# Kernel optimization log

Measured on AMD Instinct MI355X. Metric: run time of the kernel, lower is better.

## Reference

```python
import jax, jax.numpy as jnp
import numpy as np

N = 50000
E = 800000
IN, HID, OUT = 256, 128, 64
NEG_SLOPE = 0.2


def _gat(x, src, dst, W, a_src, a_dst, b, heads, dim, concat):
    # PyG GATConv (eval mode, self-loops already appended to src/dst)
    xh = (x @ W).reshape(N, heads, dim)              # [N,H,D]
    s_src = jnp.einsum('nhd,hd->nh', xh, a_src)       # [N,H]
    s_dst = jnp.einsum('nhd,hd->nh', xh, a_dst)
    e = jax.nn.leaky_relu(s_src[src] + s_dst[dst], NEG_SLOPE)  # [Etot,H]
    m = jax.ops.segment_max(e, dst, num_segments=N)
    e = jnp.exp(e - m[dst])
    z = jax.ops.segment_sum(e, dst, num_segments=N)
    alpha = e / z[dst]                                # segment softmax over incoming edges
    msg = xh[src] * alpha[:, :, None]                 # [Etot,H,D] gather + weight
    out = jax.ops.segment_sum(msg, dst, num_segments=N)  # scatter-add aggregate
    out = out.reshape(N, heads * dim) if concat else out.mean(axis=1)
    return out + b


def setup_inputs():
    key = jax.random.key(0)
    ks = jax.random.split(key, 20)
    sc = 0.05
    inp = {
        'x': jax.random.normal(ks[0], (N, IN), jnp.float32),
        'edge_index': jax.random.randint(ks[1], (2, E), 0, N, jnp.int64) if jax.config.read('jax_enable_x64') else jax.random.randint(ks[1], (2, E), 0, N, jnp.int32),
        # semantic MLP
        'w1': jax.random.normal(ks[2], (IN, HID), jnp.float32) * sc,
        'b1': jnp.zeros((HID,), jnp.float32),
        'w2': jax.random.normal(ks[3], (HID, HID), jnp.float32) * sc,
        'b2': jnp.zeros((HID,), jnp.float32),
        # gat1: HID -> HID//2, heads=4, concat -> 2*HID
        'g1_w': jax.random.normal(ks[4], (HID, 4 * (HID // 2)), jnp.float32) * sc,
        'g1_asrc': jax.random.normal(ks[5], (4, HID // 2), jnp.float32) * sc,
        'g1_adst': jax.random.normal(ks[6], (4, HID // 2), jnp.float32) * sc,
        'g1_b': jnp.zeros((2 * HID,), jnp.float32),
        # gat2: 2*HID -> OUT, heads=2, mean
        'g2_w': jax.random.normal(ks[7], (2 * HID, 2 * OUT), jnp.float32) * sc,
        'g2_asrc': jax.random.normal(ks[8], (2, OUT), jnp.float32) * sc,
        'g2_adst': jax.random.normal(ks[9], (2, OUT), jnp.float32) * sc,
        'g2_b': jnp.zeros((OUT,), jnp.float32),
        # gat3: OUT -> OUT, heads=1, mean
        'g3_w': jax.random.normal(ks[10], (OUT, OUT), jnp.float32) * sc,
        'g3_asrc': jax.random.normal(ks[11], (1, OUT), jnp.float32) * sc,
        'g3_adst': jax.random.normal(ks[12], (1, OUT), jnp.float32) * sc,
        'g3_b': jnp.zeros((OUT,), jnp.float32),
    }
    return inp


def reference(x, edge_index, w1, b1, w2, b2,
              g1_w, g1_asrc, g1_adst, g1_b,
              g2_w, g2_asrc, g2_adst, g2_b,
              g3_w, g3_asrc, g3_adst, g3_b):
    # add self loops once (PyG GATConv default add_self_loops=True)
    loop = jnp.arange(N, dtype=edge_index.dtype)
    src = jnp.concatenate([edge_index[0], loop])
    dst = jnp.concatenate([edge_index[1], loop])
    # semantic MLP (eval: dropout is identity)
    h = jax.nn.relu(x @ w1 + b1)
    h = jax.nn.relu(h @ w2 + b2)
    h = jax.nn.elu(_gat(h, src, dst, g1_w, g1_asrc, g1_adst, g1_b, 4, HID // 2, True))
    h = jax.nn.elu(_gat(h, src, dst, g2_w, g2_asrc, g2_adst, g2_b, 2, OUT, False))
    h = _gat(h, src, dst, g3_w, g3_asrc, g3_adst, g3_b, 1, OUT, False)
    return h
```

## Files before the change

kernel.cpp:

```cpp
#include <hip/hip_runtime.h>
#include <hip/hip_fp16.h>
#include <math.h>

#define NN 50000
#define NE 800000

static inline int ceil_div_h(int a, int b) { return (a + b - 1) / b; }

typedef _Float16 half8 __attribute__((ext_vector_type(8)));
typedef float f32x4 __attribute__((ext_vector_type(4)));

__global__ __launch_bounds__(256)
void convert_all_kernel(const float* __restrict__ w1, const float* __restrict__ w2,
                        const float* __restrict__ g1w, const float* __restrict__ g2w,
                        const float* __restrict__ g3w, __half* __restrict__ wt) {
  int idx = blockIdx.x * 256 + threadIdx.x;
  const float* W; int K, N, li;
  if (idx < 32768)        { W = w1;  K = 256; N = 128; li = idx; }
  else if (idx < 49152)   { W = w2;  K = 128; N = 128; li = idx - 32768; }
  else if (idx < 81920)   { W = g1w; K = 128; N = 256; li = idx - 49152; }
  else if (idx < 114688)  { W = g2w; K = 256; N = 128; li = idx - 81920; }
  else if (idx < 118784)  { W = g3w; K = 64;  N = 64;  li = idx - 114688; }
  else return;
  int n = li / K, k = li - n * K;
  wt[idx] = __float2half_rn(W[(size_t)k * N + n]);
}

template<int TN, int ACT, int OUTH, int AF32, int HS>
__global__ __launch_bounds__(256)
void mfma_gemm(const void* __restrict__ Av, const __half* __restrict__ Bt,
               const float* __restrict__ bias, void* __restrict__ Cv,
               const float* __restrict__ a_src, const float* __restrict__ a_dst,
               float* __restrict__ s_src, float* __restrict__ s_dst,
               int M, int N, int K) {
  constexpr int FM = 4;
  constexpr int FN = TN / 32;
  constexpr int SA = 40;
  __shared__ __align__(16) _Float16 As[128 * SA];
  __shared__ __align__(16) _Float16 Bs[TN * SA];
  const int tid = threadIdx.x;
  const int bm = blockIdx.y * 128, bn = blockIdx.x * TN;
  const int wave = tid >> 6, lane = tid & 63;
  const int wm = (wave & 1) * 64;
  const int wn = (wave >> 1) * (TN / 2);
  const int l16 = lane & 15, quad = lane >> 4;

  f32x4 acc[FM][FN] = {};

  for (int k0 = 0; k0 < K; k0 += 32) {
    if (AF32) {
      const float* A = (const float*)Av;
      #pragma unroll
      for (int i = 0; i < 4; ++i) {
        int idx = tid + i * 256;
        int m = idx >> 3, q = idx & 7;
        int gm = bm + m;
        float4 v = make_float4(0.f, 0.f, 0.f, 0.f);
        if (gm < M) v = *(const float4*)&A[(size_t)gm * K + k0 + q * 4];
        union { __half2 h2[2]; float2 f2; } u;
        u.h2[0] = __floats2half2_rn(v.x, v.y);
        u.h2[1] = __floats2half2_rn(v.z, v.w);
        *(float2*)&As[m * SA + q * 4] = u.f2;
      }
    } else {
      const __half* A = (const __half*)Av;
      #pragma unroll
      for (int i = 0; i < 2; ++i) {
        int idx = tid + i * 256;
        int m = idx >> 2, q = (idx & 3) * 8;
        int gm = bm + m;
        float4 raw = make_float4(0.f, 0.f, 0.f, 0.f);
        if (gm < M) raw = *(const float4*)&A[(size_t)gm * K + k0 + q];
        *(float4*)&As[m * SA + q] = raw;
      }
    }
    #pragma unroll
    for (int i = 0; i < (TN * 32) / (256 * 8); ++i) {
      int idx = tid + i * 256;
      int n = idx >> 2, kq = (idx & 3) * 8;
      float4 raw = *(const float4*)&Bt[(size_t)(bn + n) * K + k0 + kq];
      *(float4*)&Bs[n * SA + kq] = raw;
    }
    __syncthreads();
    half8 af[FM], bf[FN];
    #pragma unroll
    for (int mi = 0; mi < FM; ++mi)
      af[mi] = *(const half8*)&As[(wm + mi * 16 + l16) * SA + quad * 8];
    #pragma unroll
    for (int ni = 0; ni < FN; ++ni)
      bf[ni] = *(const half8*)&Bs[(wn + ni * 16 + l16) * SA + quad * 8];
    #pragma unroll
    for (int mi = 0; mi < FM; ++mi)
      #pragma unroll
      for (int ni = 0; ni < FN; ++ni)
        acc[mi][ni] = __builtin_amdgcn_mfma_f32_16x16x32_f16(af[mi], bf[ni], acc[mi][ni], 0, 0, 0);
    __syncthreads();
  }

  #pragma unroll
  for (int mi = 0; mi < FM; ++mi) {
    #pragma unroll
    for (int r = 0; r < 4; ++r) {
      int gm = bm + wm + mi * 16 + quad * 4 + r;
      if (gm >= M) continue;
      #pragma unroll
      for (int ni = 0; ni < FN; ++ni) {
        int gn = bn + wn + ni * 16 + l16;
        float v = acc[mi][ni][r];
        if (bias) v += bias[gn];
        if (ACT == 1) v = fmaxf(v, 0.f);
        if (OUTH) ((__half*)Cv)[(size_t)gm * N + gn] = __float2half_rn(v);
        else      ((float*)Cv)[(size_t)gm * N + gn] = v;
      }
    }
  }

  if (HS > 0) {
    const int h = (bn + wn) >> 6;
    float asv[FN], adv[FN];
    #pragma unroll
    for (int ni = 0; ni < FN; ++ni) {
      int d = ni * 16 + l16;
      asv[ni] = a_src[h * 64 + d];
      adv[ni] = a_dst[h * 64 + d];
    }
    #pragma unroll
    for (int mi = 0; mi < FM; ++mi) {
      #pragma unroll
      for (int r = 0; r < 4; ++r) {
        float ss = 0.f, sd = 0.f;
        #pragma unroll
        for (int ni = 0; ni < FN; ++ni) {
          float v = acc[mi][ni][r];
          ss = fmaf(v, asv[ni], ss);
          sd = fmaf(v, adv[ni], sd);
        }
        #pragma unroll
        for (int off = 1; off < 16; off <<= 1) {
          ss += __shfl_xor(ss, off, 64);
          sd += __shfl_xor(sd, off, 64);
        }
        int gm = bm + wm + mi * 16 + quad * 4 + r;
        if (l16 == 0 && gm < M) {
          s_src[gm * HS + h] = ss;
          s_dst[gm * HS + h] = sd;
        }
      }
    }
  }
}

template<int H>
__global__ __launch_bounds__(256)
void scores_kernel(const __half* __restrict__ xh,
                   const float* __restrict__ a_src, const float* __restrict__ a_dst,
                   float* __restrict__ s_src, float* __restrict__ s_dst) {
  const int n = (blockIdx.x * blockDim.x + threadIdx.x) >> 6;
  const int lane = threadIdx.x & 63;
  if (n >= NN) return;
  float ps[H], pd[H];
  #pragma unroll
  for (int h = 0; h < H; ++h) {
    float v = __half2float(xh[(size_t)n * (H * 64) + h * 64 + lane]);
    ps[h] = v * a_src[h * 64 + lane];
    pd[h] = v * a_dst[h * 64 + lane];
  }
  #pragma unroll
  for (int h = 0; h < H; ++h) {
    #pragma unroll
    for (int off = 32; off > 0; off >>= 1) {
      ps[h] += __shfl_xor(ps[h], off, 64);
      pd[h] += __shfl_xor(pd[h], off, 64);
    }
  }
  if (lane == 0) {
    #pragma unroll
    for (int h = 0; h < H; ++h) {
      s_src[n * H + h] = ps[h];
      s_dst[n * H + h] = pd[h];
    }
  }
}


__global__ __launch_bounds__(256)
void hist_kernel(const int* __restrict__ ei, int* __restrict__ cnt) {
  int e = blockIdx.x * blockDim.x + threadIdx.x;
  if (e >= NE) return;
  atomicAdd(&cnt[ei[NE + e]], 1);
}

__global__ __launch_bounds__(256)
void scan1_kernel(const int* __restrict__ in, int* __restrict__ out,
                  int* __restrict__ bsum, int n) {
  __shared__ int tmp[256];
  int t = threadIdx.x;
  int i = blockIdx.x * 256 + t;
  int v = (i < n) ? in[i] : 0;
  tmp[t] = v;
  __syncthreads();
  for (int off = 1; off < 256; off <<= 1) {
    int u = (t >= off) ? tmp[t - off] : 0;
    __syncthreads();
    tmp[t] += u;
    __syncthreads();
  }
  if (i <= n) out[i] = tmp[t] - v;
  if (t == 255) bsum[blockIdx.x] = tmp[255];
}

__global__ __launch_bounds__(256)
void scan2_kernel(int* __restrict__ data, int n) {
  __shared__ int tmp[256];
  int t = threadIdx.x;
  int v = (t < n) ? data[t] : 0;
  tmp[t] = v;
  __syncthreads();
  for (int off = 1; off < 256; off <<= 1) {
    int u = (t >= off) ? tmp[t - off] : 0;
    __syncthreads();
    tmp[t] += u;
    __syncthreads();
  }
  if (t < n) data[t] = tmp[t] - v;
}

__global__ __launch_bounds__(256)
void scan3_kernel(int* __restrict__ out, const int* __restrict__ bsum, int n) {
  int i = blockIdx.x * 256 + threadIdx.x;
  if (i <= n) out[i] += bsum[blockIdx.x];
}

__global__ __launch_bounds__(256)
void copy_cursor_kernel(const int* __restrict__ rowptr, int* __restrict__ cursor) {
  int i = blockIdx.x * blockDim.x + threadIdx.x;
  if (i < NN) cursor[i] = rowptr[i];
}

__global__ __launch_bounds__(256)
void scatter_kernel(const int* __restrict__ ei, int* __restrict__ cursor,
                    int* __restrict__ srcs) {
  int e = blockIdx.x * blockDim.x + threadIdx.x;
  if (e >= NE) return;
  int s = ei[e], d = ei[NE + e];
  int pos = atomicAdd(&cursor[d], 1);
  srcs[pos] = s;
}

template<int H, int MODE>
__global__ __launch_bounds__(256)
void gat_aggregate(const int* __restrict__ rowptr, const int* __restrict__ srcs,
                   const float* __restrict__ ssrc, const float* __restrict__ sdst,
                   const __half* __restrict__ xh, const float* __restrict__ bias,
                   void* __restrict__ outv) {
  constexpr int HD = H * 64;
  __shared__ float wbuf[4][64 * H];
  __shared__ int sbuf[4][64];
  const int wslot = threadIdx.x >> 6;
  const int wid = (blockIdx.x * blockDim.x + threadIdx.x) >> 6;
  const int lane = threadIdx.x & 63;
  if (wid >= NN) return;
  const int n = wid;
  const int start = rowptr[n];
  const int end = rowptr[n + 1];
  const int h = (lane * H) >> 6;

  float sdv[H];
  #pragma unroll
  for (int hh = 0; hh < H; ++hh) sdv[hh] = sdst[n * H + hh];

  float z;
  float acc[H];
  {
    float wself[H];
    #pragma unroll
    for (int hh = 0; hh < H; ++hh) {
      float e = ssrc[n * H + hh] + sdv[hh];
      e = e >= 0.f ? e : 0.2f * e;
      wself[hh] = __expf(e);
    }
    float ws = wself[h];
    z = ws;
    const __half* xr = xh + (size_t)n * HD + lane * H;
    if (H == 4) {
      float2 raw = *(const float2*)xr;
      __half2 p0 = *(__half2*)&raw.x;
      __half2 p1 = *(__half2*)&raw.y;
      float2 f0 = __half22float2(p0), f1 = __half22float2(p1);
      acc[0] = ws * f0.x; acc[1] = ws * f0.y; acc[2] = ws * f1.x; acc[3] = ws * f1.y;
    } else if (H == 2) {
      float2 f0 = __half22float2(*(const __half2*)xr);
      acc[0] = ws * f0.x; acc[1] = ws * f0.y;
    } else {
      acc[0] = ws * __half2float(xr[0]);
    }
  }

  for (int base = start; base < end; base += 64) {
    int cnt = end - base;
    if (cnt > 64) cnt = 64;
    if (lane < cnt) {
      int s = srcs[base + lane];
      sbuf[wslot][lane] = s;
      float ev[H];
      if (H == 4) {
        float4 t = *(const float4*)&ssrc[s * 4];
        ev[0] = t.x; ev[1] = t.y; ev[2] = t.z; ev[3] = t.w;
      } else if (H == 2) {
        float2 t = *(const float2*)&ssrc[s * 2];
        ev[0] = t.x; ev[1] = t.y;
      } else {
        ev[0] = ssrc[s];
      }
      #pragma unroll
      for (int hh = 0; hh < H; ++hh) {
        float e = ev[hh] + sdv[hh];
        e = e >= 0.f ? e : 0.2f * e;
        wbuf[wslot][lane * H + hh] = __expf(e);
      }
    }
    #pragma unroll 4
    for (int j = 0; j < cnt; ++j) {
      int s = sbuf[wslot][j];
      float w = wbuf[wslot][j * H + h];
      z += w;
      const __half* xr = xh + (size_t)s * HD + lane * H;
      if (H == 4) {
        float2 raw = *(const float2*)xr;
        __half2 p0 = *(__half2*)&raw.x;
        __half2 p1 = *(__half2*)&raw.y;
        float2 f0 = __half22float2(p0), f1 = __half22float2(p1);
        acc[0] = fmaf(w, f0.x, acc[0]); acc[1] = fmaf(w, f0.y, acc[1]);
        acc[2] = fmaf(w, f1.x, acc[2]); acc[3] = fmaf(w, f1.y, acc[3]);
      } else if (H == 2) {
        float2 f0 = __half22float2(*(const __half2*)xr);
        acc[0] = fmaf(w, f0.x, acc[0]); acc[1] = fmaf(w, f0.y, acc[1]);
      } else {
        acc[0] = fmaf(w, __half2float(xr[0]), acc[0]);
      }
    }
  }
  const float inv = 1.f / z;

  if (MODE == 0) {
    __half* out = (__half*)outv;
    float v[4];
    #pragma unroll
    for (int i = 0; i < 4; ++i) {
      v[i] = acc[i] * inv + bias[lane * 4 + i];
      v[i] = v[i] > 0.f ? v[i] : expm1f(v[i]);
    }
    union { __half2 h2[2]; float2 f2; } u;
    u.h2[0] = __floats2half2_rn(v[0], v[1]);
    u.h2[1] = __floats2half2_rn(v[2], v[3]);
    *(float2*)&out[(size_t)n * 256 + lane * 4] = u.f2;
  } else if (MODE == 1) {
    __half* out = (__half*)outv;
    float sv[2];
    #pragma unroll
    for (int i = 0; i < 2; ++i) {
      float mine = acc[i] * inv;
      float other = __shfl_xor(mine, 32, 64);
      sv[i] = (mine + other) * 0.5f;
    }
    if (lane < 32) {
      float v0 = sv[0] + bias[lane * 2 + 0];
      float v1 = sv[1] + bias[lane * 2 + 1];
      v0 = v0 > 0.f ? v0 : expm1f(v0);
      v1 = v1 > 0.f ? v1 : expm1f(v1);
      *(__half2*)&out[(size_t)n * 64 + lane * 2] = __floats2half2_rn(v0, v1);
    }
  } else {
    float* out = (float*)outv;
    out[(size_t)n * 64 + lane] = acc[0] * inv + bias[lane];
  }
}


extern "C" void kernel_launch(void* const* d_in, const int* in_sizes, int n_in,
                              void* d_out, int out_size, void* d_ws, size_t ws_size,
                              hipStream_t stream) {
  const float* x    = (const float*)d_in[0];
  const int*   ei   = (const int*)d_in[1];
  const float* w1   = (const float*)d_in[2];
  const float* b1   = (const float*)d_in[3];
  const float* w2   = (const float*)d_in[4];
  const float* b2   = (const float*)d_in[5];
  const float* g1w  = (const float*)d_in[6];
  const float* g1as = (const float*)d_in[7];
  const float* g1ad = (const float*)d_in[8];
  const float* g1b  = (const float*)d_in[9];
  const float* g2w  = (const float*)d_in[10];
  const float* g2as = (const float*)d_in[11];
  const float* g2ad = (const float*)d_in[12];
  const float* g2b  = (const float*)d_in[13];
  const float* g3w  = (const float*)d_in[14];
  const float* g3as = (const float*)d_in[15];
  const float* g3ad = (const float*)d_in[16];
  const float* g3b  = (const float*)d_in[17];
  float* out = (float*)d_out;

  float* ws   = (float*)d_ws;
  float* bufA = ws;
  float* bufB = bufA + (size_t)NN * 256;
  float* bufC = bufB + (size_t)NN * 256;
  float* ssrc = bufC + (size_t)NN * 256;
  float* sdst = ssrc + (size_t)NN * 4;
  int* rowptr = (int*)(sdst + (size_t)NN * 4);
  int* cursor = rowptr + (NN + 1);
  int* bsum   = cursor + NN;
  int* srcs   = bsum + 256;
  __half* wt   = (__half*)(srcs + NE);
  __half* wt1  = wt;
  __half* wt2  = wt + 32768;
  __half* wtg1 = wt + 49152;
  __half* wtg2 = wt + 81920;
  __half* wtg3 = wt + 114688;

  __half* h1  = (__half*)bufA;
  __half* h2  = (__half*)bufB;
  __half* xh1 = (__half*)bufC;
  __half* a1  = (__half*)bufA;
  __half* xh2 = (__half*)bufB;
  __half* a2  = (__half*)bufC;
  __half* xh3 = (__half*)bufB;

  const int TB = 256;
  const int grid_m = ceil_div_h(NN, 128);
  const int egrid = ceil_div_h(NE, TB);
  const int sgrid = ceil_div_h(NN + 1, TB);
  const int wgrid = ceil_div_h(NN, 4);

  convert_all_kernel<<<ceil_div_h(118784, TB), TB, 0, stream>>>(w1, w2, g1w, g2w, g3w, wt);

  hipMemsetAsync(cursor, 0, (size_t)NN * sizeof(int), stream);
  hist_kernel<<<egrid, TB, 0, stream>>>(ei, cursor);
  scan1_kernel<<<sgrid, TB, 0, stream>>>(cursor, rowptr, bsum, NN);
  scan2_kernel<<<1, TB, 0, stream>>>(bsum, sgrid);
  scan3_kernel<<<sgrid, TB, 0, stream>>>(rowptr, bsum, NN);
  copy_cursor_kernel<<<ceil_div_h(NN, TB), TB, 0, stream>>>(rowptr, cursor);
  scatter_kernel<<<egrid, TB, 0, stream>>>(ei, cursor, srcs);

  mfma_gemm<128, 1, 1, 1, 0><<<dim3(1, grid_m), TB, 0, stream>>>(
      x, wt1, b1, h1, nullptr, nullptr, nullptr, nullptr, NN, 128, 256);
  mfma_gemm<128, 1, 1, 0, 0><<<dim3(1, grid_m), TB, 0, stream>>>(
      h1, wt2, b2, h2, nullptr, nullptr, nullptr, nullptr, NN, 128, 128);

  mfma_gemm<128, 0, 1, 0, 4><<<dim3(2, grid_m), TB, 0, stream>>>(
      h2, wtg1, nullptr, xh1, g1as, g1ad, ssrc, sdst, NN, 256, 128);
  gat_aggregate<4, 0><<<wgrid, TB, 0, stream>>>(rowptr, srcs, ssrc, sdst, xh1, g1b, a1);

  mfma_gemm<128, 0, 1, 0, 2><<<dim3(1, grid_m), TB, 0, stream>>>(
      a1, wtg2, nullptr, xh2, g2as, g2ad, ssrc, sdst, NN, 128, 256);
  gat_aggregate<2, 1><<<wgrid, TB, 0, stream>>>(rowptr, srcs, ssrc, sdst, xh2, g2b, a2);

  mfma_gemm<64, 0, 1, 0, 0><<<dim3(1, grid_m), TB, 0, stream>>>(
      a2, wtg3, nullptr, xh3, nullptr, nullptr, nullptr, nullptr, NN, 64, 64);
  scores_kernel<1><<<wgrid, TB, 0, stream>>>(xh3, g3as, g3ad, ssrc, sdst);
  gat_aggregate<1, 2><<<wgrid, TB, 0, stream>>>(rowptr, srcs, ssrc, sdst, xh3, g3b, out);
}
```

Baseline: 457.8 us.

## Shrink GEMM row tiles, fuse layer-3 scores into GEMM, merge prep kernels

Makes the MFMA GEMM template take its block-M and wave layout as parameters and switches every GEMM to 64-row tiles, doubling the grid for better CU occupancy. The third-layer score computation moves into the GEMM epilogue (HS=1), which removes the separate scores kernel. The cursor memset is folded into the weight conversion kernel, and the cursor copy is folded into scan3, cutting launch count. Smaller tiles re-read the B operand more often per output row.

```diff
diff --git a/kernel.cpp b/kernel.cpp
--- a/kernel.cpp
+++ b/kernel.cpp
@@ -11,10 +11,12 @@
 typedef float f32x4 __attribute__((ext_vector_type(4)));
 
 __global__ __launch_bounds__(256)
-void convert_all_kernel(const float* __restrict__ w1, const float* __restrict__ w2,
-                        const float* __restrict__ g1w, const float* __restrict__ g2w,
-                        const float* __restrict__ g3w, __half* __restrict__ wt) {
+void prep_kernel(const float* __restrict__ w1, const float* __restrict__ w2,
+                 const float* __restrict__ g1w, const float* __restrict__ g2w,
+                 const float* __restrict__ g3w, __half* __restrict__ wt,
+                 int* __restrict__ cursor) {
   int idx = blockIdx.x * 256 + threadIdx.x;
+  if (idx < NN) cursor[idx] = 0;
   const float* W; int K, N, li;
   if (idx < 32768)        { W = w1;  K = 256; N = 128; li = idx; }
   else if (idx < 49152)   { W = w2;  K = 128; N = 128; li = idx - 32768; }
@@ -26,23 +28,23 @@
   wt[idx] = __float2half_rn(W[(size_t)k * N + n]);
 }
 
-template<int TN, int ACT, int OUTH, int AF32, int HS>
+template<int BM, int TN, int WR, int WC, int ACT, int OUTH, int AF32, int HS>
 __global__ __launch_bounds__(256)
 void mfma_gemm(const void* __restrict__ Av, const __half* __restrict__ Bt,
                const float* __restrict__ bias, void* __restrict__ Cv,
                const float* __restrict__ a_src, const float* __restrict__ a_dst,
                float* __restrict__ s_src, float* __restrict__ s_dst,
                int M, int N, int K) {
-  constexpr int FM = 4;
-  constexpr int FN = TN / 32;
+  constexpr int FM = BM / WR / 16;
+  constexpr int FN = TN / WC / 16;
   constexpr int SA = 40;
-  __shared__ __align__(16) _Float16 As[128 * SA];
+  __shared__ __align__(16) _Float16 As[BM * SA];
   __shared__ __align__(16) _Float16 Bs[TN * SA];
   const int tid = threadIdx.x;
-  const int bm = blockIdx.y * 128, bn = blockIdx.x * TN;
+  const int bm = blockIdx.y * BM, bn = blockIdx.x * TN;
   const int wave = tid >> 6, lane = tid & 63;
-  const int wm = (wave & 1) * 64;
-  const int wn = (wave >> 1) * (TN / 2);
+  const int wm = (wave % WR) * (BM / WR);
+  const int wn = (wave / WR) * (TN / WC);
   const int l16 = lane & 15, quad = lane >> 4;
 
   f32x4 acc[FM][FN] = {};
@@ -51,7 +53,7 @@
     if (AF32) {
       const float* A = (const float*)Av;
       #pragma unroll
-      for (int i = 0; i < 4; ++i) {
+      for (int i = 0; i < (BM * 8) / 256; ++i) {
         int idx = tid + i * 256;
         int m = idx >> 3, q = idx & 7;
         int gm = bm + m;
@@ -65,7 +67,7 @@
     } else {
       const __half* A = (const __half*)Av;
       #pragma unroll
-      for (int i = 0; i < 2; ++i) {
+      for (int i = 0; i < (BM * 4) / 256; ++i) {
         int idx = tid + i * 256;
         int m = idx >> 2, q = (idx & 3) * 8;
         int gm = bm + m;
@@ -75,7 +77,7 @@
       }
     }
     #pragma unroll
-    for (int i = 0; i < (TN * 32) / (256 * 8); ++i) {
+    for (int i = 0; i < (TN * 4) / 256; ++i) {
       int idx = tid + i * 256;
       int n = idx >> 2, kq = (idx & 3) * 8;
       float4 raw = *(const float4*)&Bt[(size_t)(bn + n) * K + k0 + kq];
@@ -150,38 +152,6 @@
   }
 }
 
-template<int H>
-__global__ __launch_bounds__(256)
-void scores_kernel(const __half* __restrict__ xh,
-                   const float* __restrict__ a_src, const float* __restrict__ a_dst,
-                   float* __restrict__ s_src, float* __restrict__ s_dst) {
-  const int n = (blockIdx.x * blockDim.x + threadIdx.x) >> 6;
-  const int lane = threadIdx.x & 63;
-  if (n >= NN) return;
-  float ps[H], pd[H];
-  #pragma unroll
-  for (int h = 0; h < H; ++h) {
-    float v = __half2float(xh[(size_t)n * (H * 64) + h * 64 + lane]);
-    ps[h] = v * a_src[h * 64 + lane];
-    pd[h] = v * a_dst[h * 64 + lane];
-  }
-  #pragma unroll
-  for (int h = 0; h < H; ++h) {
-    #pragma unroll
-    for (int off = 32; off > 0; off >>= 1) {
-      ps[h] += __shfl_xor(ps[h], off, 64);
-      pd[h] += __shfl_xor(pd[h], off, 64);
-    }
-  }
-  if (lane == 0) {
-    #pragma unroll
-    for (int h = 0; h < H; ++h) {
-      s_src[n * H + h] = ps[h];
-      s_dst[n * H + h] = pd[h];
-    }
-  }
-}
-
 
 __global__ __launch_bounds__(256)
 void hist_kernel(const int* __restrict__ ei, int* __restrict__ cnt) {
@@ -226,15 +196,13 @@
 }
 
 __global__ __launch_bounds__(256)
-void scan3_kernel(int* __restrict__ out, const int* __restrict__ bsum, int n) {
+void scan3_kernel(int* __restrict__ out, const int* __restrict__ bsum,
+                  int* __restrict__ cursor, int n) {
   int i = blockIdx.x * 256 + threadIdx.x;
-  if (i <= n) out[i] += bsum[blockIdx.x];
-}
-
-__global__ __launch_bounds__(256)
-void copy_cursor_kernel(const int* __restrict__ rowptr, int* __restrict__ cursor) {
-  int i = blockIdx.x * blockDim.x + threadIdx.x;
-  if (i < NN) cursor[i] = rowptr[i];
+  if (i > n) return;
+  int v = out[i] + bsum[blockIdx.x];
+  out[i] = v;
+  if (i < n) cursor[i] = v;
 }
 
 __global__ __launch_bounds__(256)
@@ -426,36 +394,33 @@
   __half* xh3 = (__half*)bufB;
 
   const int TB = 256;
-  const int grid_m = ceil_div_h(NN, 128);
+  const int grid_m = ceil_div_h(NN, 64);
   const int egrid = ceil_div_h(NE, TB);
   const int sgrid = ceil_div_h(NN + 1, TB);
   const int wgrid = ceil_div_h(NN, 4);
 
-  convert_all_kernel<<<ceil_div_h(118784, TB), TB, 0, stream>>>(w1, w2, g1w, g2w, g3w, wt);
-
-  hipMemsetAsync(cursor, 0, (size_t)NN * sizeof(int), stream);
+  prep_kernel<<<ceil_div_h(118784, TB), TB, 0, stream>>>(w1, w2, g1w, g2w, g3w, wt, cursor);
+
   hist_kernel<<<egrid, TB, 0, stream>>>(ei, cursor);
   scan1_kernel<<<sgrid, TB, 0, stream>>>(cursor, rowptr, bsum, NN);
   scan2_kernel<<<1, TB, 0, stream>>>(bsum, sgrid);
-  scan3_kernel<<<sgrid, TB, 0, stream>>>(rowptr, bsum, NN);
-  copy_cursor_kernel<<<ceil_div_h(NN, TB), TB, 0, stream>>>(rowptr, cursor);
+  scan3_kernel<<<sgrid, TB, 0, stream>>>(rowptr, bsum, cursor, NN);
   scatter_kernel<<<egrid, TB, 0, stream>>>(ei, cursor, srcs);
 
-  mfma_gemm<128, 1, 1, 1, 0><<<dim3(1, grid_m), TB, 0, stream>>>(
+  mfma_gemm<64, 128, 2, 2, 1, 1, 1, 0><<<dim3(1, grid_m), TB, 0, stream>>>(
       x, wt1, b1, h1, nullptr, nullptr, nullptr, nullptr, NN, 128, 256);
-  mfma_gemm<128, 1, 1, 0, 0><<<dim3(1, grid_m), TB, 0, stream>>>(
+  mfma_gemm<64, 128, 2, 2, 1, 1, 0, 0><<<dim3(1, grid_m), TB, 0, stream>>>(
       h1, wt2, b2, h2, nullptr, nullptr, nullptr, nullptr, NN, 128, 128);
 
-  mfma_gemm<128, 0, 1, 0, 4><<<dim3(2, grid_m), TB, 0, stream>>>(
+  mfma_gemm<64, 128, 2, 2, 0, 1, 0, 4><<<dim3(2, grid_m), TB, 0, stream>>>(
       h2, wtg1, nullptr, xh1, g1as, g1ad, ssrc, sdst, NN, 256, 128);
   gat_aggregate<4, 0><<<wgrid, TB, 0, stream>>>(rowptr, srcs, ssrc, sdst, xh1, g1b, a1);
 
-  mfma_gemm<128, 0, 1, 0, 2><<<dim3(1, grid_m), TB, 0, stream>>>(
+  mfma_gemm<64, 128, 2, 2, 0, 1, 0, 2><<<dim3(1, grid_m), TB, 0, stream>>>(
       a1, wtg2, nullptr, xh2, g2as, g2ad, ssrc, sdst, NN, 128, 256);
   gat_aggregate<2, 1><<<wgrid, TB, 0, stream>>>(rowptr, srcs, ssrc, sdst, xh2, g2b, a2);
 
-  mfma_gemm<64, 0, 1, 0, 0><<<dim3(1, grid_m), TB, 0, stream>>>(
-      a2, wtg3, nullptr, xh3, nullptr, nullptr, nullptr, nullptr, NN, 64, 64);
-  scores_kernel<1><<<wgrid, TB, 0, stream>>>(xh3, g3as, g3ad, ssrc, sdst);
+  mfma_gemm<64, 64, 4, 1, 0, 1, 0, 1><<<dim3(1, grid_m), TB, 0, stream>>>(
+      a2, wtg3, nullptr, xh3, g3as, g3ad, ssrc, sdst, NN, 64, 64);
   gat_aggregate<1, 2><<<wgrid, TB, 0, stream>>>(rowptr, srcs, ssrc, sdst, xh3, g3b, out);
 }
```

After: 417.5 us. -8.8%, faster.
